# Kernel tuning notes

Measured on AMD Instinct MI355X. Metric: run time of the kernel, lower is better.

Reference implementation:

```python
import jax, jax.numpy as jnp
import numpy as np
import math

HIDDEN = 1024
HEADS = 16
HEAD_DIM = HIDDEN // HEADS


def setup_inputs() -> dict:
    key = jax.random.key(0)
    ks = jax.random.split(key, 9)
    B, T, C = 4, 2048, HIDDEN
    s = 0.02
    x = jax.random.normal(ks[0], (B, T, C), dtype=jnp.float32)
    # torch nn.Linear weights are [out_features, in_features]
    Wq = jax.random.normal(ks[1], (C, C), dtype=jnp.float32) * s
    Wk = jax.random.normal(ks[2], (C, C), dtype=jnp.float32) * s
    Wv = jax.random.normal(ks[3], (C, C), dtype=jnp.float32) * s
    Wo = jax.random.normal(ks[4], (C, C), dtype=jnp.float32) * s
    bq = jax.random.normal(ks[5], (C,), dtype=jnp.float32) * s
    bk = jax.random.normal(ks[6], (C,), dtype=jnp.float32) * s
    bv = jax.random.normal(ks[7], (C,), dtype=jnp.float32) * s
    bo = jax.random.normal(ks[8], (C,), dtype=jnp.float32) * s
    return {"x": x, "Wq": Wq, "bq": bq, "Wk": Wk, "bk": bk,
            "Wv": Wv, "bv": bv, "Wo": Wo, "bo": bo}


def reference(x, Wq, bq, Wk, bk, Wv, bv, Wo, bo):
    B, T, C = x.shape
    H, D = HEADS, HEAD_DIM
    # projections: torch Linear => x @ W.T + b
    q = (x @ Wq.T + bq).reshape(B, T, H, D).transpose(0, 2, 1, 3)  # [B,H,T,D]
    k = (x @ Wk.T + bk).reshape(B, T, H, D).transpose(0, 2, 1, 3)
    v = (x @ Wv.T + bv).reshape(B, T, H, D).transpose(0, 2, 1, 3)
    scale = 1.0 / math.sqrt(D)
    scores = jnp.einsum('bhqd,bhkd->bhqk', q, k) * scale  # [B,H,T,T]
    attn = jax.nn.softmax(scores, axis=-1)
    y = jnp.einsum('bhqk,bhkd->bhqd', attn, v)  # [B,H,T,D]
    y = y.transpose(0, 2, 1, 3).reshape(B, T, C)
    return y @ Wo.T + bo
```

## Files before the change

kernel.cpp:

```cpp
#include <hip/hip_runtime.h>
#include <stdint.h>


using u16 = unsigned short;
using u32 = unsigned int;
typedef __attribute__((ext_vector_type(8)))  __bf16 bf16x8;
typedef __attribute__((ext_vector_type(4)))  float  floatx4;
typedef __attribute__((ext_vector_type(16))) float  f32x16;
typedef __attribute__((ext_vector_type(2)))  unsigned int u32x2;

#define QSCALE 0.18033688011112043f

__device__ __forceinline__ u16 f2b(float f) {
    union { float f; u32 i; } x; x.f = f;
    return (u16)((x.i + 0x7fffu + ((x.i >> 16) & 1u)) >> 16);
}
__device__ __forceinline__ u32 fbits(float f) { union { float f; u32 i; } x; x.f = f; return x.i; }
__device__ __forceinline__ u32 pkbf(float a, float b) {
    u32 ia = fbits(a) + 0x8000u, ib = fbits(b) + 0x8000u;
    return __builtin_amdgcn_perm(ib, ia, 0x07060302u);
}
__device__ __forceinline__ u32 cvtpk(float a, float b) {
    u32 r; asm("v_cvt_pk_bf16_f32 %0, %1, %2" : "=v"(r) : "v"(a), "v"(b)); return r;
}
__device__ __forceinline__ bf16x8 ld16B(const u16* p) {
    bf16x8 v; __builtin_memcpy(&v, p, 16); return v;
}
__device__ __forceinline__ void async16(const u16* g, u16* l) {
    __builtin_amdgcn_global_load_lds((const __attribute__((address_space(1))) unsigned int*)g,
                                     (__attribute__((address_space(3))) unsigned int*)l,
                                     16, 0, 0);
}

__global__ __launch_bounds__(256) void convert_kernel(
    const float* __restrict__ x,
    const float* __restrict__ Wq, const float* __restrict__ Wk,
    const float* __restrict__ Wv, const float* __restrict__ Wo,
    u16* __restrict__ xb, u16* __restrict__ wqb, u16* __restrict__ wkb,
    u16* __restrict__ wvb, u16* __restrict__ wob)
{
    size_t e = ((size_t)blockIdx.x * 256 + threadIdx.x) * 4;
    const float* src; u16* dst; size_t off;
    const size_t XN = (size_t)8 << 20;
    if (e < XN) { src = x; dst = xb; off = e; }
    else {
        size_t k = e - XN;
        int w = (int)(k >> 20);
        off = k & ((1u << 20) - 1);
        src = (w == 0) ? Wq : (w == 1) ? Wk : (w == 2) ? Wv : Wo;
        dst = (w == 0) ? wqb : (w == 1) ? wkb : (w == 2) ? wvb : wob;
    }
    float4 f = *(const float4*)(src + off);
    u32 dws[2] = { pkbf(f.x, f.y), pkbf(f.z, f.w) };
    __builtin_memcpy(dst + off, dws, 8);
}

__device__ __forceinline__ void gemm_loop(const u16* __restrict__ A, const u16* __restrict__ W,
                                          int m0, int n0, floatx4 (&acc)[4][4],
                                          u16* __restrict__ sA, u16* __restrict__ sB)
{
    constexpr int K = 1024;
    const int tid  = threadIdx.x;
    const int wave = tid >> 6, lane = tid & 63;
    const int wr = wave >> 1, wc = wave & 1;
    const int quad = lane >> 4, l15 = lane & 15;

    #pragma unroll
    for (int i = 0; i < 4; ++i)
        #pragma unroll
        for (int j = 0; j < 4; ++j)
            acc[i][j] = (floatx4){0.f, 0.f, 0.f, 0.f};

    const int rstage = lane >> 3;
    const int gstage = lane & 7;

    #pragma unroll 1
    for (int kb = 0; kb < 16; ++kb) {
        __syncthreads();
        const int k0 = kb * 64;
        #pragma unroll
        for (int j = 0; j < 4; ++j) {
            int r  = wave * 32 + j * 8 + rstage;
            int kg = gstage ^ (r & 7);
            async16(A + (size_t)(m0 + r) * K + k0 + kg * 8, &sA[(wave * 32 + j * 8) * 64]);
            async16(W + (size_t)(n0 + r) * K + k0 + kg * 8, &sB[(wave * 32 + j * 8) * 64]);
        }
        __syncthreads();

        #pragma unroll
        for (int kk = 0; kk < 2; ++kk) {
            bf16x8 af[4], bf[4];
            const int kg = kk * 4 + quad;
            #pragma unroll
            for (int t = 0; t < 4; ++t) {
                int ra = wr * 64 + t * 16 + l15;
                af[t] = ld16B(&sA[ra * 64 + ((kg ^ (ra & 7)) * 8)]);
                int rb = wc * 64 + t * 16 + l15;
                bf[t] = ld16B(&sB[rb * 64 + ((kg ^ (rb & 7)) * 8)]);
            }
            #pragma unroll
            for (int mt = 0; mt < 4; ++mt)
                #pragma unroll
                for (int nt = 0; nt < 4; ++nt)
                    acc[mt][nt] = __builtin_amdgcn_mfma_f32_16x16x32_bf16(af[mt], bf[nt], acc[mt][nt], 0, 0, 0);
        }
    }
}

__global__ __launch_bounds__(256, 3) void qkv_kernel(
    const u16* __restrict__ x, const u16* __restrict__ Wcat,
    const float* __restrict__ bq, const float* __restrict__ bk, const float* __restrict__ bv,
    u16* __restrict__ q, u16* __restrict__ k, u16* __restrict__ vt)
{
    __shared__ __align__(16) u16 sA[128 * 64];
    __shared__ __align__(16) u16 sB[128 * 64];
    const int id = blockIdx.x;
    const int xcd = id & 7, slot = id >> 3;
    const int m0 = (xcd * 8 + (slot & 7)) * 128;
    const int n0 = (slot >> 3) * 128;
    floatx4 acc[4][4];
    gemm_loop(x, Wcat, m0, n0, acc, sA, sB);

    const int tid = threadIdx.x;
    const int wave = tid >> 6, lane = tid & 63;
    const int wr = wave >> 1, wc = wave & 1;
    const int quad = lane >> 4, l15 = lane & 15;

    const int z = n0 >> 10;
    const float* bb = (z == 0) ? bq : (z == 1) ? bk : bv;
    const float scale = (z == 0) ? QSCALE : 1.0f;
    u16* o = (z == 0) ? q : k;

    #pragma unroll
    for (int nt = 0; nt < 4; ++nt) {
        int col  = n0 + wc * 64 + nt * 16 + l15;
        int c    = col & 1023;
        float bv_ = bb[c];
        #pragma unroll
        for (int mt = 0; mt < 4; ++mt) {
            int row0 = m0 + wr * 64 + mt * 16 + quad * 4;
            if (z == 2) {
                float v0 = acc[mt][nt][0] + bv_, v1 = acc[mt][nt][1] + bv_;
                float v2 = acc[mt][nt][2] + bv_, v3 = acc[mt][nt][3] + bv_;
                u32 dws[2] = { pkbf(v0, v1), pkbf(v2, v3) };
                int b = row0 >> 11, t0 = row0 & 2047;
                size_t idx = ((size_t)((b * 16 + (c >> 6)) * 64 + (c & 63)) * 2048) + t0;
                __builtin_memcpy(vt + idx, dws, 8);
            } else {
                #pragma unroll
                for (int r = 0; r < 4; ++r) {
                    float v = (acc[mt][nt][r] + bv_) * scale;
                    o[(size_t)(row0 + r) * 1024 + c] = f2b(v);
                }
            }
        }
    }
}

__global__ __launch_bounds__(256, 3) void proj_kernel(
    const u16* __restrict__ y, const u16* __restrict__ Wo, const float* __restrict__ bo,
    float* __restrict__ out)
{
    __shared__ __align__(16) u16 sA[128 * 64];
    __shared__ __align__(16) u16 sB[128 * 64];
    const int id = blockIdx.x;
    const int xcd = id & 7, slot = id >> 3;
    const int m0 = (xcd * 8 + (slot & 7)) * 128;
    const int n0 = (slot >> 3) * 128;
    floatx4 acc[4][4];
    gemm_loop(y, Wo, m0, n0, acc, sA, sB);

    const int tid = threadIdx.x;
    const int wave = tid >> 6, lane = tid & 63;
    const int wr = wave >> 1, wc = wave & 1;
    const int quad = lane >> 4, l15 = lane & 15;

    #pragma unroll
    for (int nt = 0; nt < 4; ++nt) {
        int col = n0 + wc * 64 + nt * 16 + l15;
        float bv_ = bo[col];
        #pragma unroll
        for (int mt = 0; mt < 4; ++mt) {
            int row0 = m0 + wr * 64 + mt * 16 + quad * 4;
            #pragma unroll
            for (int r = 0; r < 4; ++r)
                out[(size_t)(row0 + r) * 1024 + col] = acc[mt][nt][r] + bv_;
        }
    }
}

__global__ __launch_bounds__(256, 2) void attn_kernel(
    const u16* __restrict__ Q, const u16* __restrict__ K,
    const u16* __restrict__ Vt, u16* __restrict__ Y)
{
    const int bh = blockIdx.x, qt = blockIdx.y;
    const int tid = threadIdx.x;
    const int wave = tid >> 6, lane = tid & 63;
    const int hf = lane >> 5, l31 = lane & 31, l7 = l31 & 7;
    const int b = bh >> 4, h = bh & 15;

    __shared__ __align__(16) u16 smem[16384];

    bf16x8 qf[2][4];
    {
        const size_t q0 = (size_t)(b * 2048 + qt * 256 + wave * 64) * 1024 + h * 64 + hf * 8;
        #pragma unroll
        for (int nq = 0; nq < 2; ++nq)
            #pragma unroll
            for (int dc = 0; dc < 4; ++dc)
                qf[nq][dc] = ld16B(Q + q0 + (size_t)(nq * 32 + l31) * 1024 + dc * 16);
    }

    const int r8 = lane >> 3;
    const int g7 = (lane & 7) ^ r8;
    const u16* ksrc = K  + (size_t)(b * 2048 + wave * 16 + r8) * 1024 + h * 64 + g7 * 8;
    const u16* vsrc = Vt + ((size_t)(bh * 64 + wave * 16 + r8)) * 2048 + g7 * 8;

    f32x16 accO[2][2];
    #pragma unroll
    for (int dt = 0; dt < 2; ++dt)
        #pragma unroll
        for (int nq = 0; nq < 2; ++nq)
            #pragma unroll
            for (int i = 0; i < 16; ++i) accO[dt][nq][i] = 0.f;
    float accS[2] = {0.f, 0.f};

    {
        u16* dK = smem + wave * 1024;
        u16* dV = smem + 8192 + wave * 1024;
        async16(ksrc,            dK);
        async16(ksrc + 8 * 1024, dK + 512);
        async16(vsrc,            dV);
        async16(vsrc + 8 * 2048, dV + 512);
    }
    __syncthreads();

    #pragma unroll 1
    for (int kt = 0; kt < 32; ++kt) {
        const int cur = kt & 1;
        if (kt < 31) {
            u16* dK = smem + (cur ^ 1) * 4096 + wave * 1024;
            u16* dV = smem + 8192 + (cur ^ 1) * 4096 + wave * 1024;
            const u16* ks = ksrc + (size_t)(kt + 1) * 64 * 1024;
            const u16* vs = vsrc + (size_t)(kt + 1) * 64;
            async16(ks,            dK);
            async16(ks + 8 * 1024, dK + 512);
            async16(vs,            dV);
            async16(vs + 8 * 2048, dV + 512);
        }
        const u16* bK = smem + cur * 4096;
        const u16* bV = smem + 8192 + cur * 4096;

        bf16x8 kfm[2][4];
        #pragma unroll
        for (int m = 0; m < 2; ++m) {
            const int row = m * 32 + l31;
            #pragma unroll
            for (int dc = 0; dc < 4; ++dc)
                kfm[m][dc] = ld16B(&bK[row * 64 + (((dc * 2 + hf) ^ l7) * 8)]);
        }

        f32x16 st[2][2];
        #pragma unroll
        for (int m = 0; m < 2; ++m)
            #pragma unroll
            for (int nq = 0; nq < 2; ++nq)
                #pragma unroll
                for (int i = 0; i < 16; ++i) st[m][nq][i] = 0.f;
        __builtin_amdgcn_s_setprio(1);
        #pragma unroll
        for (int dc = 0; dc < 4; ++dc)
            #pragma unroll
            for (int m = 0; m < 2; ++m)
                #pragma unroll
                for (int nq = 0; nq < 2; ++nq)
                    st[m][nq] = __builtin_amdgcn_mfma_f32_32x32x16_bf16(kfm[m][dc], qf[nq][dc], st[m][nq], 0, 0, 0);
        __builtin_amdgcn_s_setprio(0);

        bf16x8 vfm[2][4];
        #pragma unroll
        for (int dt = 0; dt < 2; ++dt) {
            const int row = dt * 32 + l31;
            #pragma unroll
            for (int c = 0; c < 4; ++c)
                vfm[dt][c] = ld16B(&bV[row * 64 + (((c * 2 + hf) ^ l7) * 8)]);
        }

        #pragma unroll
        for (int c = 0; c < 4; ++c) {
            const int m = c >> 1, r0 = (c & 1) * 8;
            #pragma unroll
            for (int nq = 0; nq < 2; ++nq) {
                float e0 = __builtin_amdgcn_exp2f(st[m][nq][r0 + 0]);
                float e1 = __builtin_amdgcn_exp2f(st[m][nq][r0 + 1]);
                float e2 = __builtin_amdgcn_exp2f(st[m][nq][r0 + 2]);
                float e3 = __builtin_amdgcn_exp2f(st[m][nq][r0 + 3]);
                float e4 = __builtin_amdgcn_exp2f(st[m][nq][r0 + 4]);
                float e5 = __builtin_amdgcn_exp2f(st[m][nq][r0 + 5]);
                float e6 = __builtin_amdgcn_exp2f(st[m][nq][r0 + 6]);
                float e7 = __builtin_amdgcn_exp2f(st[m][nq][r0 + 7]);
                accS[nq] += ((e0 + e1) + (e2 + e3)) + ((e4 + e5) + (e6 + e7));
                u32 Ua = cvtpk(e0, e1), Ub = cvtpk(e2, e3);
                u32 Va = cvtpk(e4, e5), Vb = cvtpk(e6, e7);
                u32x2 s0 = __builtin_amdgcn_permlane32_swap(Ua, Va, false, false);
                u32x2 s1 = __builtin_amdgcn_permlane32_swap(Ub, Vb, false, false);
                u32 dws[4] = { s0.x, s1.x, s0.y, s1.y };
                bf16x8 pB; __builtin_memcpy(&pB, dws, 16);
                __builtin_amdgcn_s_setprio(1);
                accO[0][nq] = __builtin_amdgcn_mfma_f32_32x32x16_bf16(vfm[0][c], pB, accO[0][nq], 0, 0, 0);
                accO[1][nq] = __builtin_amdgcn_mfma_f32_32x32x16_bf16(vfm[1][c], pB, accO[1][nq], 0, 0, 0);
                __builtin_amdgcn_s_setprio(0);
            }
        }
        __syncthreads();
    }

    #pragma unroll
    for (int nq = 0; nq < 2; ++nq) accS[nq] += __shfl_xor(accS[nq], 32);
    const float inv0 = 1.f / accS[0], inv1 = 1.f / accS[1];

    u16* ep = smem + wave * 4096;
    #pragma unroll
    for (int nq = 0; nq < 2; ++nq) {
        const float inv = nq ? inv1 : inv0;
        const int row = nq * 32 + l31;
        #pragma unroll
        for (int dt = 0; dt < 2; ++dt)
            #pragma unroll
            for (int rq = 0; rq < 4; ++rq) {
                float v0 = accO[dt][nq][rq * 4 + 0] * inv;
                float v1 = accO[dt][nq][rq * 4 + 1] * inv;
                float v2 = accO[dt][nq][rq * 4 + 2] * inv;
                float v3 = accO[dt][nq][rq * 4 + 3] * inv;
                u32 dws[2] = { cvtpk(v0, v1), cvtpk(v2, v3) };
                const int g = dt * 4 + rq;
                __builtin_memcpy((char*)ep + row * 128 + ((g ^ l7) * 16) + hf * 8, dws, 8);
            }
    }
    const int rl = lane >> 3, cl = lane & 7;
    #pragma unroll
    for (int pass = 0; pass < 8; ++pass) {
        const int row = pass * 8 + rl;
        bf16x8 vrow = ld16B((const u16*)((const char*)ep + row * 128 + ((cl ^ rl) * 16)));
        const int t = qt * 256 + wave * 64 + row;
        __builtin_memcpy(Y + ((size_t)(b * 2048 + t)) * 1024 + h * 64 + cl * 8, &vrow, 16);
    }
}

extern "C" void kernel_launch(void* const* d_in, const int* in_sizes, int n_in,
                              void* d_out, int out_size, void* d_ws, size_t ws_size,
                              hipStream_t stream)
{
    const float* x  = (const float*)d_in[0];
    const float* Wq = (const float*)d_in[1];
    const float* bq = (const float*)d_in[2];
    const float* Wk = (const float*)d_in[3];
    const float* bk = (const float*)d_in[4];
    const float* Wv = (const float*)d_in[5];
    const float* bv = (const float*)d_in[6];
    const float* Wo = (const float*)d_in[7];
    const float* bo = (const float*)d_in[8];
    float* out = (float*)d_out;

    const size_t NTOK = (size_t)8192 * 1024;
    const size_t WN   = (size_t)1024 * 1024;
    u16* xb  = (u16*)d_ws;
    u16* wqb = xb + NTOK;
    u16* wkb = wqb + WN;
    u16* wvb = wkb + WN;
    u16* wob = wvb + WN;
    u16* q   = wob + WN;
    u16* k   = q + NTOK;
    u16* vt  = k + NTOK;
    u16* y   = vt + NTOK;

    convert_kernel<<<dim3(12288), 256, 0, stream>>>(x, Wq, Wk, Wv, Wo, xb, wqb, wkb, wvb, wob);
    qkv_kernel<<<dim3(1536), 256, 0, stream>>>(xb, wqb, bq, bk, bv, q, k, vt);
    attn_kernel<<<dim3(64, 8), 256, 0, stream>>>(q, k, vt, y);
    proj_kernel<<<dim3(512), 256, 0, stream>>>(y, wob, bo, out);
}
```

Before: 263.7 us.

## Give each wave private K/V LDS buffers to drop block-wide barriers

The attention kernel now gives each wave its own private K and V tiles in LDS, doubling the shared allocation. It drops the cooperative, double-buffered load and its per-iteration __syncthreads. Each wave waits on its own vmcnt, reads fragments into registers, then issues the next tile's async loads into the same buffer, overlapping them with the MFMA and exp work. This removes block-level synchronisation but makes every wave load the full K/V tile itself, quadrupling global/L2 traffic per block. The larger LDS footprint may also lower occupancy.

```diff
diff --git a/kernel.cpp b/kernel.cpp
--- a/kernel.cpp
+++ b/kernel.cpp
@@ -199,7 +199,9 @@
     const int hf = lane >> 5, l31 = lane & 31, l7 = l31 & 7;
     const int b = bh >> 4, h = bh & 15;
 
-    __shared__ __align__(16) u16 smem[16384];
+    __shared__ __align__(16) u16 smem[32768];
+    u16* mK = smem + wave * 8192;
+    u16* mV = mK + 4096;
 
     bf16x8 qf[2][4];
     {
@@ -213,8 +215,8 @@
 
     const int r8 = lane >> 3;
     const int g7 = (lane & 7) ^ r8;
-    const u16* ksrc = K  + (size_t)(b * 2048 + wave * 16 + r8) * 1024 + h * 64 + g7 * 8;
-    const u16* vsrc = Vt + ((size_t)(bh * 64 + wave * 16 + r8)) * 2048 + g7 * 8;
+    const u16* kbase = K  + (size_t)(b * 2048 + r8) * 1024 + h * 64 + g7 * 8;
+    const u16* vbase = Vt + ((size_t)(bh * 64 + r8)) * 2048 + g7 * 8;
 
     f32x16 accO[2][2];
     #pragma unroll
@@ -224,32 +226,18 @@
             #pragma unroll
             for (int i = 0; i < 16; ++i) accO[dt][nq][i] = 0.f;
     float accS[2] = {0.f, 0.f};
-
-    {
-        u16* dK = smem + wave * 1024;
-        u16* dV = smem + 8192 + wave * 1024;
-        async16(ksrc,            dK);
-        async16(ksrc + 8 * 1024, dK + 512);
-        async16(vsrc,            dV);
-        async16(vsrc + 8 * 2048, dV + 512);
-    }
-    __syncthreads();
+    const f32x16 fz = {0.f,0.f,0.f,0.f,0.f,0.f,0.f,0.f,0.f,0.f,0.f,0.f,0.f,0.f,0.f,0.f};
+
+    #pragma unroll
+    for (int i = 0; i < 8; ++i) {
+        async16(kbase + (size_t)(i * 8) * 1024, mK + i * 512);
+        async16(vbase + (size_t)(i * 8) * 2048, mV + i * 512);
+    }
 
     #pragma unroll 1
     for (int kt = 0; kt < 32; ++kt) {
-        const int cur = kt & 1;
-        if (kt < 31) {
-            u16* dK = smem + (cur ^ 1) * 4096 + wave * 1024;
-            u16* dV = smem + 8192 + (cur ^ 1) * 4096 + wave * 1024;
-            const u16* ks = ksrc + (size_t)(kt + 1) * 64 * 1024;
-            const u16* vs = vsrc + (size_t)(kt + 1) * 64;
-            async16(ks,            dK);
-            async16(ks + 8 * 1024, dK + 512);
-            async16(vs,            dV);
-            async16(vs + 8 * 2048, dV + 512);
-        }
-        const u16* bK = smem + cur * 4096;
-        const u16* bV = smem + 8192 + cur * 4096;
+        asm volatile("s_waitcnt vmcnt(0)" ::: "memory");
+        __builtin_amdgcn_sched_barrier(0);
 
         bf16x8 kfm[2][4];
         #pragma unroll
@@ -257,19 +245,27 @@
             const int row = m * 32 + l31;
             #pragma unroll
             for (int dc = 0; dc < 4; ++dc)
-                kfm[m][dc] = ld16B(&bK[row * 64 + (((dc * 2 + hf) ^ l7) * 8)]);
+                kfm[m][dc] = ld16B(&mK[row * 64 + (((dc * 2 + hf) ^ l7) * 8)]);
+        }
+        asm volatile("s_waitcnt lgkmcnt(0)" ::: "memory");
+        __builtin_amdgcn_sched_barrier(0);
+
+        if (kt < 31) {
+            const u16* kn = kbase + (size_t)((kt + 1) * 64) * 1024;
+            #pragma unroll
+            for (int i = 0; i < 8; ++i)
+                async16(kn + (size_t)(i * 8) * 1024, mK + i * 512);
         }
 
         f32x16 st[2][2];
+        __builtin_amdgcn_s_setprio(1);
         #pragma unroll
         for (int m = 0; m < 2; ++m)
             #pragma unroll
             for (int nq = 0; nq < 2; ++nq)
-                #pragma unroll
-                for (int i = 0; i < 16; ++i) st[m][nq][i] = 0.f;
-        __builtin_amdgcn_s_setprio(1);
-        #pragma unroll
-        for (int dc = 0; dc < 4; ++dc)
+                st[m][nq] = __builtin_amdgcn_mfma_f32_32x32x16_bf16(kfm[m][0], qf[nq][0], fz, 0, 0, 0);
+        #pragma unroll
+        for (int dc = 1; dc < 4; ++dc)
             #pragma unroll
             for (int m = 0; m < 2; ++m)
                 #pragma unroll
@@ -283,7 +279,16 @@
             const int row = dt * 32 + l31;
             #pragma unroll
             for (int c = 0; c < 4; ++c)
-                vfm[dt][c] = ld16B(&bV[row * 64 + (((c * 2 + hf) ^ l7) * 8)]);
+                vfm[dt][c] = ld16B(&mV[row * 64 + (((c * 2 + hf) ^ l7) * 8)]);
+        }
+        asm volatile("s_waitcnt lgkmcnt(0)" ::: "memory");
+        __builtin_amdgcn_sched_barrier(0);
+
+        if (kt < 31) {
+            const u16* vn = vbase + (size_t)((kt + 1) * 64);
+            #pragma unroll
+            for (int i = 0; i < 8; ++i)
+                async16(vn + (size_t)(i * 8) * 2048, mV + i * 512);
         }
 
         #pragma unroll
@@ -312,14 +317,13 @@
                 __builtin_amdgcn_s_setprio(0);
             }
         }
-        __syncthreads();
     }
 
     #pragma unroll
     for (int nq = 0; nq < 2; ++nq) accS[nq] += __shfl_xor(accS[nq], 32);
     const float inv0 = 1.f / accS[0], inv1 = 1.f / accS[1];
 
-    u16* ep = smem + wave * 4096;
+    u16* ep = mK;
     #pragma unroll
     for (int nq = 0; nq < 2; ++nq) {
         const float inv = nq ? inv1 : inv0;
@@ -341,7 +345,7 @@
     #pragma unroll
     for (int pass = 0; pass < 8; ++pass) {
         const int row = pass * 8 + rl;
-        bf16x8 vrow = ld16B((const u16*)((const char*)ep + row * 128 + ((cl ^ rl) * 16)));
+        bf16x8 vrow = ld16B((const u16*)((const char*)ep + row * 128 + ((cl ^ (row & 7)) * 16)));
         const int t = qt * 256 + wave * 64 + row;
         __builtin_memcpy(Y + ((size_t)(b * 2048 + t)) * 1024 + h * 64 + cl * 8, &vrow, 16);
     }
```

Result: slower. 276.1 us (+4.7%).

## Double-buffer shared-memory tiles in GEMM loop with async prefetch

Applied to the files above, without the earlier changes.

Restructures the projection GEMM main loop into a two-stage ping-pong pipeline. The K-step shrinks from 64 to 32 so that two buffers fit in the same shared memory, and the XOR swizzle is adapted to the narrower rows. The next tile's async global-to-LDS loads are issued before the MFMAs on the current tile, and there is one barrier per step instead of two. The aim is to hide global load latency behind compute, at the cost of twice as many loop iterations with fewer MFMAs between barriers. A separate epilogue index change uses row&7 in place of rl, which gives the same value.

```diff
diff --git a/kernel.cpp b/kernel.cpp
--- a/kernel.cpp
+++ b/kernel.cpp
@@ -71,39 +71,45 @@
         for (int j = 0; j < 4; ++j)
             acc[i][j] = (floatx4){0.f, 0.f, 0.f, 0.f};
 
-    const int rstage = lane >> 3;
-    const int gstage = lane & 7;
-
+    const int rstage = lane >> 2;
+    const int gs     = (lane & 3) ^ (rstage & 3);
+
+    auto stage = [&](int buf, int ph) {
+        const int k0 = ph * 32;
+        #pragma unroll
+        for (int j = 0; j < 2; ++j) {
+            int r = wave * 32 + j * 16 + rstage;
+            async16(A + (size_t)(m0 + r) * K + k0 + gs * 8,
+                    sA + buf * 4096 + (wave * 32 + j * 16) * 32);
+            async16(W + (size_t)(n0 + r) * K + k0 + gs * 8,
+                    sB + buf * 4096 + (wave * 32 + j * 16) * 32);
+        }
+    };
+
+    stage(0, 0);
+    __syncthreads();
+
+    int buf = 0;
     #pragma unroll 1
-    for (int kb = 0; kb < 16; ++kb) {
+    for (int ph = 0; ph < 32; ++ph) {
+        if (ph < 31) stage(buf ^ 1, ph + 1);
+        const u16* bA = sA + buf * 4096;
+        const u16* bB = sB + buf * 4096;
+        bf16x8 af[4], bf[4];
+        #pragma unroll
+        for (int t = 0; t < 4; ++t) {
+            int ra = wr * 64 + t * 16 + l15;
+            af[t] = ld16B(&bA[ra * 32 + ((quad ^ (ra & 3)) * 8)]);
+            int rb = wc * 64 + t * 16 + l15;
+            bf[t] = ld16B(&bB[rb * 32 + ((quad ^ (rb & 3)) * 8)]);
+        }
+        #pragma unroll
+        for (int mt = 0; mt < 4; ++mt)
+            #pragma unroll
+            for (int nt = 0; nt < 4; ++nt)
+                acc[mt][nt] = __builtin_amdgcn_mfma_f32_16x16x32_bf16(af[mt], bf[nt], acc[mt][nt], 0, 0, 0);
         __syncthreads();
-        const int k0 = kb * 64;
-        #pragma unroll
-        for (int j = 0; j < 4; ++j) {
-            int r  = wave * 32 + j * 8 + rstage;
-            int kg = gstage ^ (r & 7);
-            async16(A + (size_t)(m0 + r) * K + k0 + kg * 8, &sA[(wave * 32 + j * 8) * 64]);
-            async16(W + (size_t)(n0 + r) * K + k0 + kg * 8, &sB[(wave * 32 + j * 8) * 64]);
-        }
-        __syncthreads();
-
-        #pragma unroll
-        for (int kk = 0; kk < 2; ++kk) {
-            bf16x8 af[4], bf[4];
-            const int kg = kk * 4 + quad;
-            #pragma unroll
-            for (int t = 0; t < 4; ++t) {
-                int ra = wr * 64 + t * 16 + l15;
-                af[t] = ld16B(&sA[ra * 64 + ((kg ^ (ra & 7)) * 8)]);
-                int rb = wc * 64 + t * 16 + l15;
-                bf[t] = ld16B(&sB[rb * 64 + ((kg ^ (rb & 7)) * 8)]);
-            }
-            #pragma unroll
-            for (int mt = 0; mt < 4; ++mt)
-                #pragma unroll
-                for (int nt = 0; nt < 4; ++nt)
-                    acc[mt][nt] = __builtin_amdgcn_mfma_f32_16x16x32_bf16(af[mt], bf[nt], acc[mt][nt], 0, 0, 0);
-        }
+        buf ^= 1;
     }
 }
 
@@ -341,7 +347,7 @@
     #pragma unroll
     for (int pass = 0; pass < 8; ++pass) {
         const int row = pass * 8 + rl;
-        bf16x8 vrow = ld16B((const u16*)((const char*)ep + row * 128 + ((cl ^ rl) * 16)));
+        bf16x8 vrow = ld16B((const u16*)((const char*)ep + row * 128 + ((cl ^ (row & 7)) * 16)));
         const int t = qt * 256 + wave * 64 + row;
         __builtin_memcpy(Y + ((size_t)(b * 2048 + t)) * 1024 + h * 64 + cl * 8, &vrow, 16);
     }
```

New measurement: 266.9 us. Within noise of the previous version (+1.2%).
